# Performance work log

Measured on AMD Instinct MI355X. Metric: run time of the kernel, lower is better.

## Reference

```python
import jax, jax.numpy as jnp
import numpy as np

B, L, E, H = 2, 2048, 1024, 16
D = E // H
EPS = 1e-5


def setup_inputs() -> dict:
    key = jax.random.key(0)
    ks = jax.random.split(key, 12)
    s = 1.0 / np.sqrt(E)
    x = jax.random.normal(ks[0], (B, L, E), dtype=jnp.float32)
    # bool mask: True = block. Causal upper-triangular mask (L, S) with S == L.
    mask = jnp.triu(jnp.ones((L, L), dtype=jnp.bool_), k=1)
    Wq = jax.random.normal(ks[1], (E, E), jnp.float32) * s
    bq = jax.random.normal(ks[2], (E,), jnp.float32) * 0.01
    Wk = jax.random.normal(ks[3], (E, E), jnp.float32) * s
    bk = jax.random.normal(ks[4], (E,), jnp.float32) * 0.01
    Wv = jax.random.normal(ks[5], (E, E), jnp.float32) * s
    bv = jax.random.normal(ks[6], (E,), jnp.float32) * 0.01
    Wo = jax.random.normal(ks[7], (E, E), jnp.float32) * s
    bo = jax.random.normal(ks[8], (E,), jnp.float32) * 0.01
    gamma = jnp.ones((E,), jnp.float32)
    beta = jnp.zeros((E,), jnp.float32)
    return {"x": x, "mask": mask, "Wq": Wq, "bq": bq, "Wk": Wk, "bk": bk,
            "Wv": Wv, "bv": bv, "Wo": Wo, "bo": bo, "gamma": gamma, "beta": beta}


def reference(x, mask, Wq, bq, Wk, bk, Wv, bv, Wo, bo, gamma, beta):
    b, l, e = x.shape
    x = jnp.nan_to_num(x, nan=0.0, posinf=1e9, neginf=-1e9)
    # QKV projections (torch Linear: x @ W.T + b), split heads -> (B,H,L,D)
    q = (x @ Wq.T + bq).reshape(b, l, H, D).transpose(0, 2, 1, 3)
    k = (x @ Wk.T + bk).reshape(b, l, H, D).transpose(0, 2, 1, 3)
    v = (x @ Wv.T + bv).reshape(b, l, H, D).transpose(0, 2, 1, 3)
    scale = max(D ** 0.5, 1e-6)
    scores = jnp.einsum('bhtd,bhsd->bhts', q, k) / scale  # (B,H,L,L)
    # bool mask True=block -> additive -inf, broadcast (L,L) over (B,H)
    scores = scores + jnp.where(mask, -jnp.inf, 0.0).astype(scores.dtype)
    scores = scores - jnp.max(scores, axis=-1, keepdims=True)
    scores = jnp.nan_to_num(scores, nan=0.0, posinf=1e9, neginf=-1e9)
    attn = jax.nn.softmax(scores, axis=-1)
    o = jnp.einsum('bhts,bhsd->bhtd', attn, v)
    o = o.transpose(0, 2, 1, 3).reshape(b, l, e)
    y = o @ Wo.T + bo
    r = y + x
    # LayerNorm over last dim
    mu = jnp.mean(r, axis=-1, keepdims=True)
    var = jnp.mean((r - mu) ** 2, axis=-1, keepdims=True)
    out = (r - mu) * jax.lax.rsqrt(var + EPS) * gamma + beta
    out = jnp.nan_to_num(out, nan=0.0, posinf=1e9, neginf=-1e9)
    return out
```

## Files before the change

### kernel.cpp

```cpp
#include <hip/hip_runtime.h>
#include <hip/hip_bf16.h>
#include <cstdint>
#include <cstddef>

#define NB 2
#define NL 2048
#define NE 1024
#define NH 16
#define ND 64
#define NM (NB * NL)

typedef float f32x4 __attribute__((ext_vector_type(4)));
typedef __bf16 bf16x8 __attribute__((ext_vector_type(8)));
typedef __bf16 bf16x4 __attribute__((ext_vector_type(4)));

#define DEV static __device__ __forceinline__

DEV f32x4 mfma16(bf16x8 a, bf16x8 b, f32x4 c) {
  return __builtin_amdgcn_mfma_f32_16x16x32_bf16(a, b, c, 0, 0, 0);
}

DEV ushort f2bf(float f) {
  uint32_t u = __float_as_uint(f);
  uint32_t r = (u + 0x7fffu + ((u >> 16) & 1u)) >> 16;
  return (ushort)r;
}

#if __has_builtin(__builtin_amdgcn_exp2f)
DEV float fast_exp2(float x) { return __builtin_amdgcn_exp2f(x); }
#else
DEV float fast_exp2(float x) { return exp2f(x); }
#endif

DEV void gl_lds16(const void* src, void* lds_dst) {
  __builtin_amdgcn_global_load_lds(
      (const __attribute__((address_space(1))) void*)src,
      (__attribute__((address_space(3))) void*)lds_dst, 16, 0, 0);
}

template <int NCALLS>
DEV void stage_swz(const char* gbase, size_t row_stride_b, char* lds_base, int tid) {
#pragma unroll
  for (int c = 0; c < NCALLS; ++c) {
    uint32_t P = (uint32_t)(c * 4096 + tid * 16);
    uint32_t r = P >> 7;
    uint32_t Lo = P ^ ((r & 7u) << 4);
    gl_lds16(gbase + (size_t)r * row_stride_b + (Lo & 127u), lds_base + P);
  }
}

DEV void stage8k_swz(const char* gbase, size_t row_stride_b, char* lds_base, int tid) {
  uint32_t P = (uint32_t)(tid * 16);
  uint32_t r = P >> 7;
  uint32_t Lo = P ^ ((r & 7u) << 4);
  gl_lds16(gbase + (size_t)r * row_stride_b + (Lo & 127u), lds_base + P);
}

__global__ __launch_bounds__(256) void pack_kernel(
    const float* __restrict__ x, const float* __restrict__ wq,
    const float* __restrict__ wk, const float* __restrict__ wv,
    const float* __restrict__ wo, ushort* __restrict__ xb,
    ushort* __restrict__ wqb, ushort* __restrict__ wkb,
    ushort* __restrict__ wvb, ushort* __restrict__ wob) {
  int64_t q = (int64_t)blockIdx.x * 256 + threadIdx.x;
  const float* src;
  ushort* dst;
  bool cl;
  if (q < 1048576) {
    src = x + q * 4;
    dst = xb + q * 4;
    cl = true;
  } else {
    int64_t r = q - 1048576;
    int wsel = (int)(r >> 18);
    int64_t o = (r & 262143) * 4;
    cl = false;
    if (wsel == 0) { src = wq + o; dst = wqb + o; }
    else if (wsel == 1) { src = wk + o; dst = wkb + o; }
    else if (wsel == 2) { src = wv + o; dst = wvb + o; }
    else { src = wo + o; dst = wob + o; }
  }
  float4 v = *(const float4*)src;
  if (cl) {
    v.x = (v.x != v.x) ? 0.f : fminf(fmaxf(v.x, -1e9f), 1e9f);
    v.y = (v.y != v.y) ? 0.f : fminf(fmaxf(v.y, -1e9f), 1e9f);
    v.z = (v.z != v.z) ? 0.f : fminf(fmaxf(v.z, -1e9f), 1e9f);
    v.w = (v.w != v.w) ? 0.f : fminf(fmaxf(v.w, -1e9f), 1e9f);
  }
  ushort4 o4;
  o4.x = f2bf(v.x);
  o4.y = f2bf(v.y);
  o4.z = f2bf(v.z);
  o4.w = f2bf(v.w);
  *(ushort4*)dst = o4;
}

__global__ __launch_bounds__(256) void qkv_gemm_kernel(
    const ushort* __restrict__ xb, const ushort* __restrict__ wqb,
    const ushort* __restrict__ wkb, const ushort* __restrict__ wvb,
    const float* __restrict__ bq, const float* __restrict__ bk,
    const float* __restrict__ bv, ushort* __restrict__ Qo,
    ushort* __restrict__ Ko, ushort* __restrict__ Vto) {
  __shared__ __align__(128) char lds[65536];
  const int tid = threadIdx.x;
  const int w = tid >> 6, ln = tid & 63;
  const int ln15 = ln & 15, g = ln >> 4;
  const int wm = w >> 1, wn = w & 1;
  const int m0 = blockIdx.y * 128;
  const int which = blockIdx.x >> 3;
  const int n0w = (blockIdx.x & 7) * 128;
  const ushort* Wb = (which == 0) ? wqb : (which == 1) ? wkb : wvb;

  const char* Abase = (const char*)xb + (size_t)m0 * 2048;
  const char* Bbase = (const char*)Wb + (size_t)n0w * 2048;

  f32x4 acc[4][4];
#pragma unroll
  for (int m = 0; m < 4; ++m)
#pragma unroll
    for (int n = 0; n < 4; ++n) acc[m][n] = {0.f, 0.f, 0.f, 0.f};

  int cur = 0;
  stage_swz<4>(Abase, 2048, lds, tid);
  stage_swz<4>(Bbase, 2048, lds + 32768, tid);

  for (int kt = 0; kt < 16; ++kt) {
    asm volatile("s_waitcnt vmcnt(0)" ::: "memory");
    __builtin_amdgcn_s_barrier();
    asm volatile("" ::: "memory");
    if (kt + 1 < 16) {
      stage_swz<4>(Abase + (kt + 1) * 128, 2048, lds + (cur ^ 1) * 16384, tid);
      stage_swz<4>(Bbase + (kt + 1) * 128, 2048,
                   lds + 32768 + (cur ^ 1) * 16384, tid);
    }
    const char* ab = lds + cur * 16384;
    const char* bb = lds + 32768 + cur * 16384;
    __builtin_amdgcn_s_setprio(1);
#pragma unroll
    for (int kc = 0; kc < 2; ++kc) {
      bf16x8 af[4], bfr[4];
#pragma unroll
      for (int i = 0; i < 4; ++i) {
        uint32_t ar = (uint32_t)(wm * 64 + i * 16 + ln15);
        uint32_t ao = (ar * 128u + (uint32_t)(kc * 64 + g * 16)) ^ ((ar & 7u) << 4);
        af[i] = *(const bf16x8*)(ab + ao);
        uint32_t br = (uint32_t)(wn * 64 + i * 16 + ln15);
        uint32_t bo_ = (br * 128u + (uint32_t)(kc * 64 + g * 16)) ^ ((br & 7u) << 4);
        bfr[i] = *(const bf16x8*)(bb + bo_);
      }
#pragma unroll
      for (int m = 0; m < 4; ++m)
#pragma unroll
        for (int n = 0; n < 4; ++n) acc[m][n] = mfma16(af[m], bfr[n], acc[m][n]);
    }
    __builtin_amdgcn_s_setprio(0);
    cur ^= 1;
  }

  const float* bias = (which == 0) ? bq : (which == 1) ? bk : bv;
  const float sc = (which == 0) ? 0.18033688011112042f : 1.0f;
#pragma unroll
  for (int n = 0; n < 4; ++n) {
    const int col = n0w + wn * 64 + n * 16 + ln15;
    const int h = col >> 6, d = col & 63;
    const float bc = bias[col];
#pragma unroll
    for (int m = 0; m < 4; ++m) {
      if (which < 2) {
        ushort* dst = (which == 0) ? Qo : Ko;
#pragma unroll
        for (int j = 0; j < 4; ++j) {
          int mg = m0 + wm * 64 + m * 16 + g * 4 + j;
          int b = mg >> 11, l = mg & 2047;
          dst[((size_t)(b * NH + h) * NL + l) * ND + d] = f2bf((acc[m][n][j] + bc) * sc);
        }
      } else {
        int mg0 = m0 + wm * 64 + m * 16 + g * 4;
        int b = mg0 >> 11, l0 = mg0 & 2047;
        ushort4 pk;
        pk.x = f2bf(acc[m][n][0] + bc);
        pk.y = f2bf(acc[m][n][1] + bc);
        pk.z = f2bf(acc[m][n][2] + bc);
        pk.w = f2bf(acc[m][n][3] + bc);
        *(ushort4*)(Vto + ((size_t)(b * NH + h) * ND + d) * NL + l0) = pk;
      }
    }
  }
}

__global__ __launch_bounds__(512) void attn_kernel(
    const ushort* __restrict__ Q, const ushort* __restrict__ K,
    const ushort* __restrict__ Vt, ushort* __restrict__ Op) {
  __shared__ __align__(128) char lds[49152];
  const int tid = threadIdx.x;
  const int w = tid >> 6, ln = tid & 63;
  const int ln15 = ln & 15, g = ln >> 4;
  const int bx = blockIdx.x;
  const int bh = bx & 31;
  const int seg = bx >> 5;
  const int qt = (seg < 8) ? 15 - seg : seg - 8;
  const int nt = 2 * qt + 2;

  const int b = bh >> 4, h = bh & 15;
  const ushort* Qh = Q + (size_t)bh * NL * ND;
  const ushort* Kh = K + (size_t)bh * NL * ND;
  const ushort* Vth = Vt + (size_t)bh * ND * NL;
  const uint32_t pbase = 32768u + (uint32_t)w * 2048u;

  const int q0 = qt * 128;
  const int r0 = q0 + w * 16;

  bf16x8 qf[2];
#pragma unroll
  for (int kc = 0; kc < 2; ++kc)
    qf[kc] = *(const bf16x8*)(Qh + (size_t)(r0 + ln15) * ND + kc * 32 + g * 8);

  f32x4 o_acc[4];
#pragma unroll
  for (int n = 0; n < 4; ++n) o_acc[n] = {0.f, 0.f, 0.f, 0.f};
  float m_run = -1e30f, l_run = 0.f;

  int cur = 0;
  stage8k_swz((const char*)Kh, 128, lds, tid);
  stage8k_swz((const char*)Vth, (size_t)NL * 2, lds + 16384, tid);

  for (int t = 0; t < nt; ++t) {
    const int s0 = t * 64;
    asm volatile("s_waitcnt vmcnt(0)" ::: "memory");
    __builtin_amdgcn_s_barrier();
    asm volatile("" ::: "memory");
    if (t + 1 < nt) {
      stage8k_swz((const char*)Kh + (size_t)(s0 + 64) * 128, 128,
                  lds + (cur ^ 1) * 8192, tid);
      stage8k_swz((const char*)Vth + (size_t)(s0 + 64) * 2, (size_t)NL * 2,
                  lds + 16384 + (cur ^ 1) * 8192, tid);
    }

    if (s0 <= r0 + 15) {
      const char* kb = lds + cur * 8192;
      const char* vb = lds + 16384 + cur * 8192;

      f32x4 s_acc[4];
#pragma unroll
      for (int n = 0; n < 4; ++n) s_acc[n] = {0.f, 0.f, 0.f, 0.f};
      __builtin_amdgcn_s_setprio(1);
#pragma unroll
      for (int kc = 0; kc < 2; ++kc) {
        bf16x8 kf[4];
#pragma unroll
        for (int n = 0; n < 4; ++n) {
          uint32_t kr = (uint32_t)(n * 16 + ln15);
          uint32_t off = (kr * 128u + (uint32_t)(kc * 64 + g * 16)) ^ ((kr & 7u) << 4);
          kf[n] = *(const bf16x8*)(kb + off);
        }
#pragma unroll
        for (int n = 0; n < 4; ++n) s_acc[n] = mfma16(kf[n], qf[kc], s_acc[n]);
      }
      __builtin_amdgcn_s_setprio(0);

      if (s0 + 63 > r0) {
        const int qi = r0 + ln15;
#pragma unroll
        for (int n = 0; n < 4; ++n)
#pragma unroll
          for (int j = 0; j < 4; ++j) {
            int si = s0 + n * 16 + g * 4 + j;
            s_acc[n][j] = (si > qi) ? -1e30f : s_acc[n][j];
          }
      }

      float mx;
      {
        float a0 = fmaxf(fmaxf(s_acc[0][0], s_acc[0][1]), s_acc[0][2]);
        float a1 = fmaxf(fmaxf(s_acc[0][3], s_acc[1][0]), s_acc[1][1]);
        float a2 = fmaxf(fmaxf(s_acc[1][2], s_acc[1][3]), s_acc[2][0]);
        float a3 = fmaxf(fmaxf(s_acc[2][1], s_acc[2][2]), s_acc[2][3]);
        float a4 = fmaxf(fmaxf(s_acc[3][0], s_acc[3][1]), s_acc[3][2]);
        float b0 = fmaxf(fmaxf(a0, a1), a2);
        float b1 = fmaxf(fmaxf(a3, a4), s_acc[3][3]);
        mx = fmaxf(b0, b1);
      }
      if (__any(mx > m_run + 8.0f)) {
        float mr = fmaxf(mx, __shfl_xor(mx, 16));
        mr = fmaxf(mr, __shfl_xor(mr, 32));
        float mn = fmaxf(m_run, mr);
        float al = fast_exp2(m_run - mn);
        m_run = mn;
        l_run *= al;
#pragma unroll
        for (int j = 0; j < 4; ++j) {
          float aj = __shfl(al, g * 4 + j);
#pragma unroll
          for (int n = 0; n < 4; ++n) o_acc[n][j] *= aj;
        }
      }
      float ps = 0.f;
#pragma unroll
      for (int n = 0; n < 4; ++n) {
        float p0 = fast_exp2(s_acc[n][0] - m_run);
        float p1 = fast_exp2(s_acc[n][1] - m_run);
        float p2 = fast_exp2(s_acc[n][2] - m_run);
        float p3 = fast_exp2(s_acc[n][3] - m_run);
        ps += (p0 + p1) + (p2 + p3);
        bf16x4 pk = {(__bf16)p0, (__bf16)p1, (__bf16)p2, (__bf16)p3};
        uint32_t off = ((uint32_t)ln15 * 128u + (uint32_t)(n * 32 + g * 8)) ^
                       (((uint32_t)ln15 & 7u) << 4);
        *(bf16x4*)(lds + pbase + off) = pk;
      }
      l_run += ps;

      __builtin_amdgcn_s_setprio(1);
#pragma unroll
      for (int kc = 0; kc < 2; ++kc) {
        uint32_t poff = ((uint32_t)ln15 * 128u + (uint32_t)(kc * 64 + g * 16)) ^
                        (((uint32_t)ln15 & 7u) << 4);
        bf16x8 pf = *(const bf16x8*)(lds + pbase + poff);
        bf16x8 vf[4];
#pragma unroll
        for (int n = 0; n < 4; ++n) {
          uint32_t vr = (uint32_t)(n * 16 + ln15);
          uint32_t off = (vr * 128u + (uint32_t)(kc * 64 + g * 16)) ^ ((vr & 7u) << 4);
          vf[n] = *(const bf16x8*)(vb + off);
        }
#pragma unroll
        for (int n = 0; n < 4; ++n) o_acc[n] = mfma16(pf, vf[n], o_acc[n]);
      }
      __builtin_amdgcn_s_setprio(0);
    }
    cur ^= 1;
  }

  l_run += __shfl_xor(l_run, 16);
  l_run += __shfl_xor(l_run, 32);

  float invl = 1.0f / l_run;
#pragma unroll
  for (int j = 0; j < 4; ++j) {
    float inv = __shfl(invl, g * 4 + j);
    int qi = r0 + g * 4 + j;
    size_t rowo = ((size_t)b * NL + qi) * NE + h * ND;
#pragma unroll
    for (int n = 0; n < 4; ++n) Op[rowo + n * 16 + ln15] = f2bf(o_acc[n][j] * inv);
  }
}

__global__ __launch_bounds__(256) void oproj_kernel(
    const ushort* __restrict__ ob, const ushort* __restrict__ wob,
    const float* __restrict__ bo, const float* __restrict__ x,
    float* __restrict__ out) {
  __shared__ __align__(128) char lds[65536];
  const int tid = threadIdx.x;
  const int w = tid >> 6, ln = tid & 63;
  const int ln15 = ln & 15, g = ln >> 4;
  const int wm = w >> 1, wn = w & 1;
  const int m0 = blockIdx.y * 128;
  const int n0 = blockIdx.x * 128;

  const char* Abase = (const char*)ob + (size_t)m0 * 2048;
  const char* Bbase = (const char*)wob + (size_t)n0 * 2048;

  f32x4 acc[4][4];
#pragma unroll
  for (int m = 0; m < 4; ++m)
#pragma unroll
    for (int n = 0; n < 4; ++n) acc[m][n] = {0.f, 0.f, 0.f, 0.f};

  int cur = 0;
  stage_swz<4>(Abase, 2048, lds, tid);
  stage_swz<4>(Bbase, 2048, lds + 32768, tid);

  for (int kt = 0; kt < 16; ++kt) {
    asm volatile("s_waitcnt vmcnt(0)" ::: "memory");
    __builtin_amdgcn_s_barrier();
    asm volatile("" ::: "memory");
    if (kt + 1 < 16) {
      stage_swz<4>(Abase + (kt + 1) * 128, 2048, lds + (cur ^ 1) * 16384, tid);
      stage_swz<4>(Bbase + (kt + 1) * 128, 2048,
                   lds + 32768 + (cur ^ 1) * 16384, tid);
    }
    const char* ab = lds + cur * 16384;
    const char* bb = lds + 32768 + cur * 16384;
    __builtin_amdgcn_s_setprio(1);
#pragma unroll
    for (int kc = 0; kc < 2; ++kc) {
      bf16x8 af[4], bfr[4];
#pragma unroll
      for (int i = 0; i < 4; ++i) {
        uint32_t ar = (uint32_t)(wm * 64 + i * 16 + ln15);
        uint32_t ao = (ar * 128u + (uint32_t)(kc * 64 + g * 16)) ^ ((ar & 7u) << 4);
        af[i] = *(const bf16x8*)(ab + ao);
        uint32_t br = (uint32_t)(wn * 64 + i * 16 + ln15);
        uint32_t bo_ = (br * 128u + (uint32_t)(kc * 64 + g * 16)) ^ ((br & 7u) << 4);
        bfr[i] = *(const bf16x8*)(bb + bo_);
      }
#pragma unroll
      for (int m = 0; m < 4; ++m)
#pragma unroll
        for (int n = 0; n < 4; ++n) acc[m][n] = mfma16(af[m], bfr[n], acc[m][n]);
    }
    __builtin_amdgcn_s_setprio(0);
    cur ^= 1;
  }

#pragma unroll
  for (int n = 0; n < 4; ++n) {
    const int col = n0 + wn * 64 + n * 16 + ln15;
    const float bc = bo[col];
#pragma unroll
    for (int m = 0; m < 4; ++m)
#pragma unroll
      for (int j = 0; j < 4; ++j) {
        int mg = m0 + wm * 64 + m * 16 + g * 4 + j;
        size_t idx = (size_t)mg * NE + col;
        out[idx] = acc[m][n][j] + bc + x[idx];
      }
  }
}

__global__ __launch_bounds__(256) void ln_kernel(float* __restrict__ io,
                                                 const float* __restrict__ gamma,
                                                 const float* __restrict__ beta) {
  const int row = blockIdx.x, tid = threadIdx.x;
  const int w = tid >> 6, ln = tid & 63;
  float4 v = *(const float4*)(io + (size_t)row * NE + tid * 4);
  float s = v.x + v.y + v.z + v.w;
  float ss = v.x * v.x + v.y * v.y + v.z * v.z + v.w * v.w;
#pragma unroll
  for (int d = 1; d < 64; d <<= 1) {
    s += __shfl_xor(s, d);
    ss += __shfl_xor(ss, d);
  }
  __shared__ float red[8];
  if (ln == 0) {
    red[w] = s;
    red[4 + w] = ss;
  }
  __syncthreads();
  s = red[0] + red[1] + red[2] + red[3];
  ss = red[4] + red[5] + red[6] + red[7];
  const float mu = s * (1.0f / (float)NE);
  float var = ss * (1.0f / (float)NE) - mu * mu;
  const float inv = rsqrtf(var + 1e-5f);
  float4 gv = *(const float4*)(gamma + tid * 4);
  float4 bv = *(const float4*)(beta + tid * 4);
  float4 o;
  o.x = (v.x - mu) * inv * gv.x + bv.x;
  o.y = (v.y - mu) * inv * gv.y + bv.y;
  o.z = (v.z - mu) * inv * gv.z + bv.z;
  o.w = (v.w - mu) * inv * gv.w + bv.w;
  *(float4*)(io + (size_t)row * NE + tid * 4) = o;
}

extern "C" void kernel_launch(void* const* d_in, const int* in_sizes, int n_in,
                              void* d_out, int out_size, void* d_ws, size_t ws_size,
                              hipStream_t stream) {
  const float* x = (const float*)d_in[0];
  const float* Wq = (const float*)d_in[2];
  const float* bq = (const float*)d_in[3];
  const float* Wk = (const float*)d_in[4];
  const float* bk = (const float*)d_in[5];
  const float* Wv = (const float*)d_in[6];
  const float* bv = (const float*)d_in[7];
  const float* Wo = (const float*)d_in[8];
  const float* bo = (const float*)d_in[9];
  const float* gamma = (const float*)d_in[10];
  const float* beta = (const float*)d_in[11];

  char* ws = (char*)d_ws;
  ushort* xb  = (ushort*)(ws + 0);
  ushort* wqb = (ushort*)(ws + 8388608);
  ushort* wkb = (ushort*)(ws + 10485760);
  ushort* wvb = (ushort*)(ws + 12582912);
  ushort* wob = (ushort*)(ws + 14680064);
  ushort* Qb  = (ushort*)(ws + 16777216);
  ushort* Kb  = (ushort*)(ws + 25165824);
  ushort* Vtb = (ushort*)(ws + 33554432);
  ushort* Ob  = (ushort*)(ws + 41943040);

  pack_kernel<<<8192, 256, 0, stream>>>(x, Wq, Wk, Wv, Wo, xb, wqb, wkb, wvb, wob);
  qkv_gemm_kernel<<<dim3(24, 32), 256, 0, stream>>>(xb, wqb, wkb, wvb, bq, bk, bv,
                                                    Qb, Kb, Vtb);
  attn_kernel<<<512, 512, 0, stream>>>(Qb, Kb, Vtb, Ob);
  oproj_kernel<<<dim3(8, 32), 256, 0, stream>>>(Ob, wob, bo, x, (float*)d_out);
  ln_kernel<<<4096, 256, 0, stream>>>((float*)d_out, gamma, beta);
}
```

Before: 105.7 us.

## Process two 16-row query tiles per wave in attention with 4-wave blocks

The attention kernel now runs 256 threads (4 waves) per block, and each wave handles 32 query rows as two 16-row MFMA tiles instead of one. Each K and V fragment loaded from LDS then feeds twice as many MFMAs, which cuts LDS read traffic per FLOP, and half as many threads issue the staging loads for each tile. The cost is roughly double the accumulator registers per wave and fewer waves per block to hide latency. The causal skip also gets coarser, so some fully masked 16-row subtiles are still computed.

```diff
diff --git a/kernel.cpp b/kernel.cpp
--- a/kernel.cpp
+++ b/kernel.cpp
@@ -47,13 +47,6 @@
     uint32_t Lo = P ^ ((r & 7u) << 4);
     gl_lds16(gbase + (size_t)r * row_stride_b + (Lo & 127u), lds_base + P);
   }
-}
-
-DEV void stage8k_swz(const char* gbase, size_t row_stride_b, char* lds_base, int tid) {
-  uint32_t P = (uint32_t)(tid * 16);
-  uint32_t r = P >> 7;
-  uint32_t Lo = P ^ ((r & 7u) << 4);
-  gl_lds16(gbase + (size_t)r * row_stride_b + (Lo & 127u), lds_base + P);
 }
 
 __global__ __launch_bounds__(256) void pack_kernel(
@@ -188,7 +181,7 @@
   }
 }
 
-__global__ __launch_bounds__(512) void attn_kernel(
+__global__ __launch_bounds__(256) void attn_kernel(
     const ushort* __restrict__ Q, const ushort* __restrict__ K,
     const ushort* __restrict__ Vt, ushort* __restrict__ Op) {
   __shared__ __align__(128) char lds[49152];
@@ -205,24 +198,29 @@
   const ushort* Qh = Q + (size_t)bh * NL * ND;
   const ushort* Kh = K + (size_t)bh * NL * ND;
   const ushort* Vth = Vt + (size_t)bh * ND * NL;
-  const uint32_t pbase = 32768u + (uint32_t)w * 2048u;
+  const uint32_t pbase = 32768u + (uint32_t)w * 4096u;
 
   const int q0 = qt * 128;
-  const int r0 = q0 + w * 16;
-
-  bf16x8 qf[2];
-#pragma unroll
-  for (int kc = 0; kc < 2; ++kc)
-    qf[kc] = *(const bf16x8*)(Qh + (size_t)(r0 + ln15) * ND + kc * 32 + g * 8);
-
-  f32x4 o_acc[4];
-#pragma unroll
-  for (int n = 0; n < 4; ++n) o_acc[n] = {0.f, 0.f, 0.f, 0.f};
-  float m_run = -1e30f, l_run = 0.f;
+  const int r0 = q0 + w * 32;
+
+  bf16x8 qf[2][2];
+#pragma unroll
+  for (int m = 0; m < 2; ++m)
+#pragma unroll
+    for (int kc = 0; kc < 2; ++kc)
+      qf[m][kc] = *(const bf16x8*)(Qh + (size_t)(r0 + m * 16 + ln15) * ND +
+                                   kc * 32 + g * 8);
+
+  f32x4 o_acc[2][4];
+#pragma unroll
+  for (int m = 0; m < 2; ++m)
+#pragma unroll
+    for (int n = 0; n < 4; ++n) o_acc[m][n] = {0.f, 0.f, 0.f, 0.f};
+  float m_run[2] = {-1e30f, -1e30f}, l_run[2] = {0.f, 0.f};
 
   int cur = 0;
-  stage8k_swz((const char*)Kh, 128, lds, tid);
-  stage8k_swz((const char*)Vth, (size_t)NL * 2, lds + 16384, tid);
+  stage_swz<2>((const char*)Kh, 128, lds, tid);
+  stage_swz<2>((const char*)Vth, (size_t)NL * 2, lds + 16384, tid);
 
   for (int t = 0; t < nt; ++t) {
     const int s0 = t * 64;
@@ -230,19 +228,21 @@
     __builtin_amdgcn_s_barrier();
     asm volatile("" ::: "memory");
     if (t + 1 < nt) {
-      stage8k_swz((const char*)Kh + (size_t)(s0 + 64) * 128, 128,
-                  lds + (cur ^ 1) * 8192, tid);
-      stage8k_swz((const char*)Vth + (size_t)(s0 + 64) * 2, (size_t)NL * 2,
-                  lds + 16384 + (cur ^ 1) * 8192, tid);
-    }
-
-    if (s0 <= r0 + 15) {
+      stage_swz<2>((const char*)Kh + (size_t)(s0 + 64) * 128, 128,
+                   lds + (cur ^ 1) * 8192, tid);
+      stage_swz<2>((const char*)Vth + (size_t)(s0 + 64) * 2, (size_t)NL * 2,
+                   lds + 16384 + (cur ^ 1) * 8192, tid);
+    }
+
+    if (s0 <= r0 + 31) {
       const char* kb = lds + cur * 8192;
       const char* vb = lds + 16384 + cur * 8192;
 
-      f32x4 s_acc[4];
-#pragma unroll
-      for (int n = 0; n < 4; ++n) s_acc[n] = {0.f, 0.f, 0.f, 0.f};
+      f32x4 s_acc[2][4];
+#pragma unroll
+      for (int m = 0; m < 2; ++m)
+#pragma unroll
+        for (int n = 0; n < 4; ++n) s_acc[m][n] = {0.f, 0.f, 0.f, 0.f};
       __builtin_amdgcn_s_setprio(1);
 #pragma unroll
       for (int kc = 0; kc < 2; ++kc) {
@@ -254,67 +254,74 @@
           kf[n] = *(const bf16x8*)(kb + off);
         }
 #pragma unroll
-        for (int n = 0; n < 4; ++n) s_acc[n] = mfma16(kf[n], qf[kc], s_acc[n]);
+        for (int m = 0; m < 2; ++m)
+#pragma unroll
+          for (int n = 0; n < 4; ++n)
+            s_acc[m][n] = mfma16(kf[n], qf[m][kc], s_acc[m][n]);
       }
       __builtin_amdgcn_s_setprio(0);
 
-      if (s0 + 63 > r0) {
-        const int qi = r0 + ln15;
-#pragma unroll
-        for (int n = 0; n < 4; ++n)
+#pragma unroll
+      for (int m = 0; m < 2; ++m) {
+        const int rm = r0 + m * 16;
+        if (s0 + 63 > rm) {
+          const int qi = rm + ln15;
+#pragma unroll
+          for (int n = 0; n < 4; ++n)
+#pragma unroll
+            for (int j = 0; j < 4; ++j) {
+              int si = s0 + n * 16 + g * 4 + j;
+              s_acc[m][n][j] = (si > qi) ? -1e30f : s_acc[m][n][j];
+            }
+        }
+        float mx;
+        {
+          float a0 = fmaxf(fmaxf(s_acc[m][0][0], s_acc[m][0][1]), s_acc[m][0][2]);
+          float a1 = fmaxf(fmaxf(s_acc[m][0][3], s_acc[m][1][0]), s_acc[m][1][1]);
+          float a2 = fmaxf(fmaxf(s_acc[m][1][2], s_acc[m][1][3]), s_acc[m][2][0]);
+          float a3 = fmaxf(fmaxf(s_acc[m][2][1], s_acc[m][2][2]), s_acc[m][2][3]);
+          float a4 = fmaxf(fmaxf(s_acc[m][3][0], s_acc[m][3][1]), s_acc[m][3][2]);
+          float b0 = fmaxf(fmaxf(a0, a1), a2);
+          float b1 = fmaxf(fmaxf(a3, a4), s_acc[m][3][3]);
+          mx = fmaxf(b0, b1);
+        }
+        if (__any(mx > m_run[m] + 8.0f)) {
+          float mr = fmaxf(mx, __shfl_xor(mx, 16));
+          mr = fmaxf(mr, __shfl_xor(mr, 32));
+          float mn = fmaxf(m_run[m], mr);
+          float al = fast_exp2(m_run[m] - mn);
+          m_run[m] = mn;
+          l_run[m] *= al;
 #pragma unroll
           for (int j = 0; j < 4; ++j) {
-            int si = s0 + n * 16 + g * 4 + j;
-            s_acc[n][j] = (si > qi) ? -1e30f : s_acc[n][j];
+            float aj = __shfl(al, g * 4 + j);
+#pragma unroll
+            for (int n = 0; n < 4; ++n) o_acc[m][n][j] *= aj;
           }
-      }
-
-      float mx;
-      {
-        float a0 = fmaxf(fmaxf(s_acc[0][0], s_acc[0][1]), s_acc[0][2]);
-        float a1 = fmaxf(fmaxf(s_acc[0][3], s_acc[1][0]), s_acc[1][1]);
-        float a2 = fmaxf(fmaxf(s_acc[1][2], s_acc[1][3]), s_acc[2][0]);
-        float a3 = fmaxf(fmaxf(s_acc[2][1], s_acc[2][2]), s_acc[2][3]);
-        float a4 = fmaxf(fmaxf(s_acc[3][0], s_acc[3][1]), s_acc[3][2]);
-        float b0 = fmaxf(fmaxf(a0, a1), a2);
-        float b1 = fmaxf(fmaxf(a3, a4), s_acc[3][3]);
-        mx = fmaxf(b0, b1);
-      }
-      if (__any(mx > m_run + 8.0f)) {
-        float mr = fmaxf(mx, __shfl_xor(mx, 16));
-        mr = fmaxf(mr, __shfl_xor(mr, 32));
-        float mn = fmaxf(m_run, mr);
-        float al = fast_exp2(m_run - mn);
-        m_run = mn;
-        l_run *= al;
-#pragma unroll
-        for (int j = 0; j < 4; ++j) {
-          float aj = __shfl(al, g * 4 + j);
-#pragma unroll
-          for (int n = 0; n < 4; ++n) o_acc[n][j] *= aj;
-        }
-      }
-      float ps = 0.f;
-#pragma unroll
-      for (int n = 0; n < 4; ++n) {
-        float p0 = fast_exp2(s_acc[n][0] - m_run);
-        float p1 = fast_exp2(s_acc[n][1] - m_run);
-        float p2 = fast_exp2(s_acc[n][2] - m_run);
-        float p3 = fast_exp2(s_acc[n][3] - m_run);
-        ps += (p0 + p1) + (p2 + p3);
-        bf16x4 pk = {(__bf16)p0, (__bf16)p1, (__bf16)p2, (__bf16)p3};
-        uint32_t off = ((uint32_t)ln15 * 128u + (uint32_t)(n * 32 + g * 8)) ^
-                       (((uint32_t)ln15 & 7u) << 4);
-        *(bf16x4*)(lds + pbase + off) = pk;
-      }
-      l_run += ps;
+        }
+        float ps = 0.f;
+#pragma unroll
+        for (int n = 0; n < 4; ++n) {
+          float p0 = fast_exp2(s_acc[m][n][0] - m_run[m]);
+          float p1 = fast_exp2(s_acc[m][n][1] - m_run[m]);
+          float p2 = fast_exp2(s_acc[m][n][2] - m_run[m]);
+          float p3 = fast_exp2(s_acc[m][n][3] - m_run[m]);
+          ps += (p0 + p1) + (p2 + p3);
+          bf16x4 pk = {(__bf16)p0, (__bf16)p1, (__bf16)p2, (__bf16)p3};
+          uint32_t off = ((uint32_t)ln15 * 128u + (uint32_t)(n * 32 + g * 8)) ^
+                         (((uint32_t)ln15 & 7u) << 4);
+          *(bf16x4*)(lds + pbase + m * 2048 + off) = pk;
+        }
+        l_run[m] += ps;
+      }
 
       __builtin_amdgcn_s_setprio(1);
 #pragma unroll
       for (int kc = 0; kc < 2; ++kc) {
         uint32_t poff = ((uint32_t)ln15 * 128u + (uint32_t)(kc * 64 + g * 16)) ^
                         (((uint32_t)ln15 & 7u) << 4);
-        bf16x8 pf = *(const bf16x8*)(lds + pbase + poff);
+        bf16x8 pf0 = *(const bf16x8*)(lds + pbase + poff);
+        bf16x8 pf1 = *(const bf16x8*)(lds + pbase + 2048 + poff);
         bf16x8 vf[4];
 #pragma unroll
         for (int n = 0; n < 4; ++n) {
@@ -323,24 +330,30 @@
           vf[n] = *(const bf16x8*)(vb + off);
         }
 #pragma unroll
-        for (int n = 0; n < 4; ++n) o_acc[n] = mfma16(pf, vf[n], o_acc[n]);
+        for (int n = 0; n < 4; ++n) {
+          o_acc[0][n] = mfma16(pf0, vf[n], o_acc[0][n]);
+          o_acc[1][n] = mfma16(pf1, vf[n], o_acc[1][n]);
+        }
       }
       __builtin_amdgcn_s_setprio(0);
     }
     cur ^= 1;
   }
 
-  l_run += __shfl_xor(l_run, 16);
-  l_run += __shfl_xor(l_run, 32);
-
-  float invl = 1.0f / l_run;
-#pragma unroll
-  for (int j = 0; j < 4; ++j) {
-    float inv = __shfl(invl, g * 4 + j);
-    int qi = r0 + g * 4 + j;
-    size_t rowo = ((size_t)b * NL + qi) * NE + h * ND;
-#pragma unroll
-    for (int n = 0; n < 4; ++n) Op[rowo + n * 16 + ln15] = f2bf(o_acc[n][j] * inv);
+#pragma unroll
+  for (int m = 0; m < 2; ++m) {
+    l_run[m] += __shfl_xor(l_run[m], 16);
+    l_run[m] += __shfl_xor(l_run[m], 32);
+    float invl = 1.0f / l_run[m];
+#pragma unroll
+    for (int j = 0; j < 4; ++j) {
+      float inv = __shfl(invl, g * 4 + j);
+      int qi = r0 + m * 16 + g * 4 + j;
+      size_t rowo = ((size_t)b * NL + qi) * NE + h * ND;
+#pragma unroll
+      for (int n = 0; n < 4; ++n)
+        Op[rowo + n * 16 + ln15] = f2bf(o_acc[m][n][j] * inv);
+    }
   }
 }
 
@@ -480,7 +493,7 @@
   pack_kernel<<<8192, 256, 0, stream>>>(x, Wq, Wk, Wv, Wo, xb, wqb, wkb, wvb, wob);
   qkv_gemm_kernel<<<dim3(24, 32), 256, 0, stream>>>(xb, wqb, wkb, wvb, bq, bk, bv,
                                                     Qb, Kb, Vtb);
-  attn_kernel<<<512, 512, 0, stream>>>(Qb, Kb, Vtb, Ob);
+  attn_kernel<<<512, 256, 0, stream>>>(Qb, Kb, Vtb, Ob);
   oproj_kernel<<<dim3(8, 32), 256, 0, stream>>>(Ob, wob, bo, x, (float*)d_out);
   ln_kernel<<<4096, 256, 0, stream>>>((float*)d_out, gamma, beta);
 }
```

After: 119.1 us. 12.6% more time.

## Single-buffer B tile via register prefetch to cut QKV GEMM LDS footprint

Applied to the files above, without the earlier changes.

The QKV GEMM now prefetches the weight (B) tile into registers and writes it to a single LDS buffer each step, while A stays double-buffered in LDS. This brings LDS use from 64KB down to 48KB, and the launch bounds now request 3 blocks per CU to raise occupancy. In exchange each k-step needs an extra barrier plus an LDS write phase, and more registers are tied up holding the prefetched B fragments, which may limit occupancy or cause spilling.

```diff
diff --git a/kernel.cpp b/kernel.cpp
--- a/kernel.cpp
+++ b/kernel.cpp
@@ -95,13 +95,53 @@
   *(ushort4*)dst = o4;
 }
 
-__global__ __launch_bounds__(256) void qkv_gemm_kernel(
+#define QKV_LOADB(R, t_)                                                      \
+  do {                                                                        \
+    _Pragma("unroll") for (int c = 0; c < 4; ++c)                             \
+        R[c] = *(const bf16x8*)(Bb + (size_t)(brow + 32 * c) * 1024 +         \
+                                (t_) * 64 + bcc * 8);                         \
+  } while (0)
+
+#define QKV_WRITEB(R)                                                         \
+  do {                                                                        \
+    _Pragma("unroll") for (int c = 0; c < 4; ++c) {                           \
+      uint32_t rr = (uint32_t)(brow + 32 * c);                                \
+      uint32_t off = (rr * 128u + (uint32_t)(bcc * 16)) ^ ((rr & 7u) << 4);   \
+      *(bf16x8*)(lds + 32768 + off) = R[c];                                   \
+    }                                                                         \
+  } while (0)
+
+#define QKV_COMP(AB)                                                          \
+  do {                                                                        \
+    const char* ab = (AB);                                                    \
+    const char* bb = lds + 32768;                                             \
+    __builtin_amdgcn_s_setprio(1);                                            \
+    _Pragma("unroll") for (int kc = 0; kc < 2; ++kc) {                        \
+      bf16x8 af[4], bfr[4];                                                   \
+      _Pragma("unroll") for (int i = 0; i < 4; ++i) {                         \
+        uint32_t ar = (uint32_t)(wm * 64 + i * 16 + ln15);                    \
+        uint32_t ao = (ar * 128u + (uint32_t)(kc * 64 + g * 16)) ^            \
+                      ((ar & 7u) << 4);                                       \
+        af[i] = *(const bf16x8*)(ab + ao);                                    \
+        uint32_t br = (uint32_t)(wn * 64 + i * 16 + ln15);                    \
+        uint32_t bo_ = (br * 128u + (uint32_t)(kc * 64 + g * 16)) ^           \
+                       ((br & 7u) << 4);                                      \
+        bfr[i] = *(const bf16x8*)(bb + bo_);                                  \
+      }                                                                       \
+      _Pragma("unroll") for (int m = 0; m < 4; ++m)                           \
+          _Pragma("unroll") for (int n = 0; n < 4; ++n)                       \
+              acc[m][n] = mfma16(af[m], bfr[n], acc[m][n]);                   \
+    }                                                                         \
+    __builtin_amdgcn_s_setprio(0);                                            \
+  } while (0)
+
+__global__ __launch_bounds__(256, 3) void qkv_gemm_kernel(
     const ushort* __restrict__ xb, const ushort* __restrict__ wqb,
     const ushort* __restrict__ wkb, const ushort* __restrict__ wvb,
     const float* __restrict__ bq, const float* __restrict__ bk,
     const float* __restrict__ bv, ushort* __restrict__ Qo,
     ushort* __restrict__ Ko, ushort* __restrict__ Vto) {
-  __shared__ __align__(128) char lds[65536];
+  __shared__ __align__(128) char lds[49152];
   const int tid = threadIdx.x;
   const int w = tid >> 6, ln = tid & 63;
   const int ln15 = ln & 15, g = ln >> 4;
@@ -112,7 +152,9 @@
   const ushort* Wb = (which == 0) ? wqb : (which == 1) ? wkb : wvb;
 
   const char* Abase = (const char*)xb + (size_t)m0 * 2048;
-  const char* Bbase = (const char*)Wb + (size_t)n0w * 2048;
+  const ushort* Bb = Wb + (size_t)n0w * 1024;
+  const int brow = tid >> 3;
+  const int bcc = tid & 7;
 
   f32x4 acc[4][4];
 #pragma unroll
@@ -120,41 +162,35 @@
 #pragma unroll
     for (int n = 0; n < 4; ++n) acc[m][n] = {0.f, 0.f, 0.f, 0.f};
 
-  int cur = 0;
+  bf16x8 br0[4], br1[4];
   stage_swz<4>(Abase, 2048, lds, tid);
-  stage_swz<4>(Bbase, 2048, lds + 32768, tid);
-
-  for (int kt = 0; kt < 16; ++kt) {
+  QKV_LOADB(br0, 0);
+
+  for (int kt = 0; kt < 16; kt += 2) {
     asm volatile("s_waitcnt vmcnt(0)" ::: "memory");
     __builtin_amdgcn_s_barrier();
     asm volatile("" ::: "memory");
+    QKV_WRITEB(br0);
     if (kt + 1 < 16) {
-      stage_swz<4>(Abase + (kt + 1) * 128, 2048, lds + (cur ^ 1) * 16384, tid);
-      stage_swz<4>(Bbase + (kt + 1) * 128, 2048,
-                   lds + 32768 + (cur ^ 1) * 16384, tid);
-    }
-    const char* ab = lds + cur * 16384;
-    const char* bb = lds + 32768 + cur * 16384;
-    __builtin_amdgcn_s_setprio(1);
-#pragma unroll
-    for (int kc = 0; kc < 2; ++kc) {
-      bf16x8 af[4], bfr[4];
-#pragma unroll
-      for (int i = 0; i < 4; ++i) {
-        uint32_t ar = (uint32_t)(wm * 64 + i * 16 + ln15);
-        uint32_t ao = (ar * 128u + (uint32_t)(kc * 64 + g * 16)) ^ ((ar & 7u) << 4);
-        af[i] = *(const bf16x8*)(ab + ao);
-        uint32_t br = (uint32_t)(wn * 64 + i * 16 + ln15);
-        uint32_t bo_ = (br * 128u + (uint32_t)(kc * 64 + g * 16)) ^ ((br & 7u) << 4);
-        bfr[i] = *(const bf16x8*)(bb + bo_);
-      }
-#pragma unroll
-      for (int m = 0; m < 4; ++m)
-#pragma unroll
-        for (int n = 0; n < 4; ++n) acc[m][n] = mfma16(af[m], bfr[n], acc[m][n]);
-    }
-    __builtin_amdgcn_s_setprio(0);
-    cur ^= 1;
+      stage_swz<4>(Abase + (kt + 1) * 128, 2048, lds + 16384, tid);
+      QKV_LOADB(br1, kt + 1);
+    }
+    asm volatile("s_waitcnt lgkmcnt(0)" ::: "memory");
+    __builtin_amdgcn_s_barrier();
+    asm volatile("" ::: "memory");
+    QKV_COMP(lds);
+    asm volatile("s_waitcnt vmcnt(0)" ::: "memory");
+    __builtin_amdgcn_s_barrier();
+    asm volatile("" ::: "memory");
+    QKV_WRITEB(br1);
+    if (kt + 2 < 16) {
+      stage_swz<4>(Abase + (kt + 2) * 128, 2048, lds, tid);
+      QKV_LOADB(br0, kt + 2);
+    }
+    asm volatile("s_waitcnt lgkmcnt(0)" ::: "memory");
+    __builtin_amdgcn_s_barrier();
+    asm volatile("" ::: "memory");
+    QKV_COMP(lds + 16384);
   }
 
   const float* bias = (which == 0) ? bq : (which == 1) ? bk : bv;
```

New measurement: 106.8 us. About the same (+1.0%).

## Retile QKV GEMM to 256x192 tiles with 512 threads and interleaved prefetch

Applied to the files above, without the earlier changes.

Rewrites the fused QKV projection GEMM to use 256x192 output tiles per 512-thread block, treating the contiguous Wq/Wk/Wv bf16 buffers as one 3072-row weight matrix so the 256 blocks match the CU count. Next-tile global-to-LDS loads are split into chunks interleaved with the MFMA phases, and A fragments are double-buffered in registers with partial lgkmcnt waits. The aim is higher arithmetic intensity per LDS byte and better overlap of loads with compute. In exchange it uses 112KB of LDS and many accumulator registers, and it depends on wqb/wkb/wvb being adjacent in the workspace.

```diff
diff --git a/kernel.cpp b/kernel.cpp
--- a/kernel.cpp
+++ b/kernel.cpp
@@ -51,6 +51,14 @@
 
 DEV void stage8k_swz(const char* gbase, size_t row_stride_b, char* lds_base, int tid) {
   uint32_t P = (uint32_t)(tid * 16);
+  uint32_t r = P >> 7;
+  uint32_t Lo = P ^ ((r & 7u) << 4);
+  gl_lds16(gbase + (size_t)r * row_stride_b + (Lo & 127u), lds_base + P);
+}
+
+DEV void stage_chunk(const char* gbase, size_t row_stride_b, char* lds_base,
+                     int tid, int c) {
+  uint32_t P = (uint32_t)(c * 8192 + tid * 16);
   uint32_t r = P >> 7;
   uint32_t Lo = P ^ ((r & 7u) << 4);
   gl_lds16(gbase + (size_t)r * row_stride_b + (Lo & 127u), lds_base + P);
@@ -95,93 +103,139 @@
   *(ushort4*)dst = o4;
 }
 
-__global__ __launch_bounds__(256) void qkv_gemm_kernel(
-    const ushort* __restrict__ xb, const ushort* __restrict__ wqb,
-    const ushort* __restrict__ wkb, const ushort* __restrict__ wvb,
+__global__ __launch_bounds__(512) void qkv_gemm_kernel(
+    const ushort* __restrict__ xb, const ushort* __restrict__ wqkv,
     const float* __restrict__ bq, const float* __restrict__ bk,
     const float* __restrict__ bv, ushort* __restrict__ Qo,
     ushort* __restrict__ Ko, ushort* __restrict__ Vto) {
-  __shared__ __align__(128) char lds[65536];
+  __shared__ __align__(128) char lds[114688];
   const int tid = threadIdx.x;
-  const int w = tid >> 6, ln = tid & 63;
+  const int ln = tid & 63;
   const int ln15 = ln & 15, g = ln >> 4;
-  const int wm = w >> 1, wn = w & 1;
-  const int m0 = blockIdx.y * 128;
-  const int which = blockIdx.x >> 3;
-  const int n0w = (blockIdx.x & 7) * 128;
-  const ushort* Wb = (which == 0) ? wqb : (which == 1) ? wkb : wvb;
+  const int wid = tid >> 6;
+  const int wr = wid >> 2, wc = wid & 3;
+  const int mt_ = blockIdx.x >> 4, nt_ = blockIdx.x & 15;
+  const int m0 = mt_ * 256, n0 = nt_ * 192;
 
   const char* Abase = (const char*)xb + (size_t)m0 * 2048;
-  const char* Bbase = (const char*)Wb + (size_t)n0w * 2048;
-
-  f32x4 acc[4][4];
-#pragma unroll
-  for (int m = 0; m < 4; ++m)
-#pragma unroll
-    for (int n = 0; n < 4; ++n) acc[m][n] = {0.f, 0.f, 0.f, 0.f};
-
-  int cur = 0;
-  stage_swz<4>(Abase, 2048, lds, tid);
-  stage_swz<4>(Bbase, 2048, lds + 32768, tid);
+  const char* Bbase = (const char*)wqkv + (size_t)n0 * 2048;
+
+  f32x4 acc[8][3];
+#pragma unroll
+  for (int mi = 0; mi < 8; ++mi)
+#pragma unroll
+    for (int ni = 0; ni < 3; ++ni) acc[mi][ni] = {0.f, 0.f, 0.f, 0.f};
+
+  stage_chunk(Abase, 2048, lds, tid, 0);
+  stage_chunk(Abase, 2048, lds, tid, 1);
+  stage_chunk(Abase, 2048, lds, tid, 2);
+  stage_chunk(Abase, 2048, lds, tid, 3);
+  stage_chunk(Bbase, 2048, lds + 65536, tid, 0);
+  stage_chunk(Bbase, 2048, lds + 65536, tid, 1);
+  stage_chunk(Bbase, 2048, lds + 65536, tid, 2);
 
   for (int kt = 0; kt < 16; ++kt) {
     asm volatile("s_waitcnt vmcnt(0)" ::: "memory");
     __builtin_amdgcn_s_barrier();
     asm volatile("" ::: "memory");
-    if (kt + 1 < 16) {
-      stage_swz<4>(Abase + (kt + 1) * 128, 2048, lds + (cur ^ 1) * 16384, tid);
-      stage_swz<4>(Bbase + (kt + 1) * 128, 2048,
-                   lds + 32768 + (cur ^ 1) * 16384, tid);
+    const char* ab = lds + (kt & 1) * 32768;
+    const char* bb = lds + 65536 + (kt & 1) * 24576;
+    const char* anx = Abase + (kt + 1) * 128;
+    const char* bnx = Bbase + (kt + 1) * 128;
+    char* a_dst = lds + ((kt + 1) & 1) * 32768;
+    char* b_dst = lds + 65536 + ((kt + 1) & 1) * 24576;
+
+    bf16x8 bfr[2][3];
+#pragma unroll
+    for (int kc = 0; kc < 2; ++kc)
+#pragma unroll
+      for (int ni = 0; ni < 3; ++ni) {
+        uint32_t br = (uint32_t)(wc * 48 + ni * 16 + ln15);
+        uint32_t off = (br * 128u + (uint32_t)(kc * 64 + g * 16)) ^ ((br & 7u) << 4);
+        bfr[kc][ni] = *(const bf16x8*)(bb + off);
+      }
+    bf16x8 afA[2][2], afB[2][2];
+#pragma unroll
+    for (int mi2 = 0; mi2 < 2; ++mi2)
+#pragma unroll
+      for (int kc = 0; kc < 2; ++kc) {
+        uint32_t ar = (uint32_t)(wr * 128 + mi2 * 16 + ln15);
+        uint32_t off = (ar * 128u + (uint32_t)(kc * 64 + g * 16)) ^ ((ar & 7u) << 4);
+        afA[mi2][kc] = *(const bf16x8*)(ab + off);
+      }
+
+#pragma unroll
+    for (int p = 0; p < 4; ++p) {
+      if (kt + 1 < 16) {
+        if (p == 0) { stage_chunk(anx, 2048, a_dst, tid, 0);
+                      stage_chunk(anx, 2048, a_dst, tid, 1); }
+        else if (p == 1) { stage_chunk(anx, 2048, a_dst, tid, 2);
+                           stage_chunk(anx, 2048, a_dst, tid, 3); }
+        else if (p == 2) { stage_chunk(bnx, 2048, b_dst, tid, 0);
+                           stage_chunk(bnx, 2048, b_dst, tid, 1); }
+        else { stage_chunk(bnx, 2048, b_dst, tid, 2); }
+      }
+      if (p < 3) {
+#pragma unroll
+        for (int mi2 = 0; mi2 < 2; ++mi2)
+#pragma unroll
+          for (int kc = 0; kc < 2; ++kc) {
+            uint32_t ar = (uint32_t)(wr * 128 + (2 * (p + 1) + mi2) * 16 + ln15);
+            uint32_t off = (ar * 128u + (uint32_t)(kc * 64 + g * 16)) ^
+                           ((ar & 7u) << 4);
+            if (p & 1) afA[mi2][kc] = *(const bf16x8*)(ab + off);
+            else       afB[mi2][kc] = *(const bf16x8*)(ab + off);
+          }
+        asm volatile("s_waitcnt lgkmcnt(4)" ::: "memory");
+      } else {
+        asm volatile("s_waitcnt lgkmcnt(0)" ::: "memory");
+      }
+      __builtin_amdgcn_sched_barrier(0);
+      __builtin_amdgcn_s_setprio(1);
+#pragma unroll
+      for (int ni = 0; ni < 3; ++ni)
+#pragma unroll
+        for (int kc = 0; kc < 2; ++kc)
+#pragma unroll
+          for (int mi2 = 0; mi2 < 2; ++mi2) {
+            if (p & 1)
+              acc[2 * p + mi2][ni] = mfma16(afB[mi2][kc], bfr[kc][ni],
+                                            acc[2 * p + mi2][ni]);
+            else
+              acc[2 * p + mi2][ni] = mfma16(afA[mi2][kc], bfr[kc][ni],
+                                            acc[2 * p + mi2][ni]);
+          }
+      __builtin_amdgcn_s_setprio(0);
     }
-    const char* ab = lds + cur * 16384;
-    const char* bb = lds + 32768 + cur * 16384;
-    __builtin_amdgcn_s_setprio(1);
-#pragma unroll
-    for (int kc = 0; kc < 2; ++kc) {
-      bf16x8 af[4], bfr[4];
-#pragma unroll
-      for (int i = 0; i < 4; ++i) {
-        uint32_t ar = (uint32_t)(wm * 64 + i * 16 + ln15);
-        uint32_t ao = (ar * 128u + (uint32_t)(kc * 64 + g * 16)) ^ ((ar & 7u) << 4);
-        af[i] = *(const bf16x8*)(ab + ao);
-        uint32_t br = (uint32_t)(wn * 64 + i * 16 + ln15);
-        uint32_t bo_ = (br * 128u + (uint32_t)(kc * 64 + g * 16)) ^ ((br & 7u) << 4);
-        bfr[i] = *(const bf16x8*)(bb + bo_);
-      }
-#pragma unroll
-      for (int m = 0; m < 4; ++m)
-#pragma unroll
-        for (int n = 0; n < 4; ++n) acc[m][n] = mfma16(af[m], bfr[n], acc[m][n]);
-    }
-    __builtin_amdgcn_s_setprio(0);
-    cur ^= 1;
-  }
-
-  const float* bias = (which == 0) ? bq : (which == 1) ? bk : bv;
-  const float sc = (which == 0) ? 0.18033688011112042f : 1.0f;
-#pragma unroll
-  for (int n = 0; n < 4; ++n) {
-    const int col = n0w + wn * 64 + n * 16 + ln15;
-    const int h = col >> 6, d = col & 63;
-    const float bc = bias[col];
-#pragma unroll
-    for (int m = 0; m < 4; ++m) {
+  }
+
+#pragma unroll
+  for (int ni = 0; ni < 3; ++ni) {
+    const int col = n0 + wc * 48 + ni * 16 + ln15;
+    const int which = col >> 10;
+    const int cw = col & 1023;
+    const int h = cw >> 6, d = cw & 63;
+    const float bc = (which == 0) ? bq[cw] : (which == 1) ? bk[cw] : bv[cw];
+    const float sc = (which == 0) ? 0.18033688011112042f : 1.0f;
+#pragma unroll
+    for (int mi = 0; mi < 8; ++mi) {
       if (which < 2) {
         ushort* dst = (which == 0) ? Qo : Ko;
 #pragma unroll
         for (int j = 0; j < 4; ++j) {
-          int mg = m0 + wm * 64 + m * 16 + g * 4 + j;
+          int mg = m0 + wr * 128 + mi * 16 + g * 4 + j;
           int b = mg >> 11, l = mg & 2047;
-          dst[((size_t)(b * NH + h) * NL + l) * ND + d] = f2bf((acc[m][n][j] + bc) * sc);
+          dst[((size_t)(b * NH + h) * NL + l) * ND + d] =
+              f2bf((acc[mi][ni][j] + bc) * sc);
         }
       } else {
-        int mg0 = m0 + wm * 64 + m * 16 + g * 4;
+        int mg0 = m0 + wr * 128 + mi * 16 + g * 4;
         int b = mg0 >> 11, l0 = mg0 & 2047;
         ushort4 pk;
-        pk.x = f2bf(acc[m][n][0] + bc);
-        pk.y = f2bf(acc[m][n][1] + bc);
-        pk.z = f2bf(acc[m][n][2] + bc);
-        pk.w = f2bf(acc[m][n][3] + bc);
+        pk.x = f2bf(acc[mi][ni][0] + bc);
+        pk.y = f2bf(acc[mi][ni][1] + bc);
+        pk.z = f2bf(acc[mi][ni][2] + bc);
+        pk.w = f2bf(acc[mi][ni][3] + bc);
         *(ushort4*)(Vto + ((size_t)(b * NH + h) * ND + d) * NL + l0) = pk;
       }
     }
@@ -478,8 +532,7 @@
   ushort* Ob  = (ushort*)(ws + 41943040);
 
   pack_kernel<<<8192, 256, 0, stream>>>(x, Wq, Wk, Wv, Wo, xb, wqb, wkb, wvb, wob);
-  qkv_gemm_kernel<<<dim3(24, 32), 256, 0, stream>>>(xb, wqb, wkb, wvb, bq, bk, bv,
-                                                    Qb, Kb, Vtb);
+  qkv_gemm_kernel<<<256, 512, 0, stream>>>(xb, wqb, bq, bk, bv, Qb, Kb, Vtb);
   attn_kernel<<<512, 512, 0, stream>>>(Qb, Kb, Vtb, Ob);
   oproj_kernel<<<dim3(8, 32), 256, 0, stream>>>(Ob, wob, bo, x, (float*)d_out);
   ln_kernel<<<4096, 256, 0, stream>>>((float*)d_out, gamma, beta);
```

Result: faster. 103.4 us (median of 3 runs) (-2.2%).
